# Kernel optimization log

Hardware: AMD Instinct MI355X
Metric: run time of the kernel (lower is better)

Reference implementation:

```python
import jax, jax.numpy as jnp
import numpy as np

N_USERS = 200000
N_ITEMS = 100000
N_NODES = N_USERS + N_ITEMS
N_EDGES = 1500000
EMBED_DIM = 64
BERT_DIM = 384
N_LAYERS = 3


def setup_inputs() -> dict:
    key = jax.random.key(0)
    ks = jax.random.split(key, 13)
    return {
        "user_emb": jax.random.normal(ks[0], (N_USERS, EMBED_DIM), jnp.float32) * 0.1,
        "item_emb": jax.random.normal(ks[1], (N_ITEMS, EMBED_DIM), jnp.float32) * 0.1,
        "gender_emb": jax.random.normal(ks[2], (3, EMBED_DIM), jnp.float32) * 0.1,
        "age_emb": jax.random.normal(ks[3], (8, EMBED_DIM), jnp.float32) * 0.1,
        "cat_emb": jax.random.normal(ks[4], (11, EMBED_DIM), jnp.float32) * 0.1,
        "bert_proj_w": jax.random.normal(ks[5], (EMBED_DIM, BERT_DIM), jnp.float32) * 0.05,
        "item_bert": jax.random.normal(ks[6], (N_ITEMS, BERT_DIM), jnp.float32),
        "adj_val": jax.random.uniform(ks[7], (N_EDGES,), jnp.float32),
        "user_gender": jax.random.randint(ks[8], (N_USERS,), 0, 3, jnp.int64 if jax.config.jax_enable_x64 else jnp.int32),
        "user_age": jax.random.randint(ks[9], (N_USERS,), 0, 8, jnp.int32),
        "item_cat": jax.random.randint(ks[10], (N_ITEMS,), 0, 11, jnp.int32),
        "adj_row": jax.random.randint(ks[11], (N_EDGES,), 0, N_NODES, jnp.int32),
        "adj_col": jax.random.randint(ks[12], (N_EDGES,), 0, N_NODES, jnp.int32),
    }


def reference(user_emb, item_emb, gender_emb, age_emb, cat_emb, bert_proj_w,
              item_bert, adj_val, user_gender, user_age, item_cat,
              adj_row, adj_col):
    n_users = user_emb.shape[0]
    n_nodes = n_users + item_emb.shape[0]

    # initial embeddings: base table + side-info gathers (+ projected BERT for items)
    u0 = user_emb + gender_emb[user_gender] + age_emb[user_age]          # [U, d]
    i0 = item_emb + cat_emb[item_cat] + item_bert @ bert_proj_w.T       # [I, d]
    all_emb = jnp.concatenate([u0, i0], axis=0)                          # [N, d]

    # COO SpMM: y[r] += val * x[c]
    def spmm(x):
        msgs = adj_val[:, None] * x[adj_col]                             # [E, d]
        return jax.ops.segment_sum(msgs, adj_row, num_segments=n_nodes)

    acc = all_emb
    x = all_emb
    for _ in range(N_LAYERS):
        x = spmm(x)
        acc = acc + x
    out = acc / (N_LAYERS + 1)                                           # mean over layer stack
    return out[:n_users], out[n_users:]
```

## Files before the change

kernel.cpp:

```cpp
#include <hip/hip_runtime.h>
#include <hip/hip_bf16.h>

#define NU 200000
#define NI 100000
#define NN 300000
#define NE 1500000
#define BD 384

#define SCAN1_BLOCKS 293
#define NBINS 293
#define CH 4096
#define P2CAP 6144
#define COLMASK 0x7FFFF

typedef __attribute__((ext_vector_type(8))) short short8;
typedef __attribute__((ext_vector_type(4))) float floatx4;

__device__ __forceinline__ void fma4(float4& a, float s, const float4& w) {
    a.x = fmaf(s, w.x, a.x);
    a.y = fmaf(s, w.y, a.y);
    a.z = fmaf(s, w.z, a.z);
    a.w = fmaf(s, w.w, a.w);
}

__device__ __forceinline__ float bf2f(unsigned short v) {
    union { unsigned int u; float f; } c; c.u = ((unsigned int)v) << 16; return c.f;
}
__device__ __forceinline__ float4 ub4f(const ushort4 v) {
    return make_float4(bf2f(v.x), bf2f(v.y), bf2f(v.z), bf2f(v.w));
}
__device__ __forceinline__ unsigned short f2bfu(float x) {
    union { __hip_bfloat16 b; unsigned short u; } c; c.b = __float2bfloat16(x); return c.u;
}
__device__ __forceinline__ ushort4 f4bf(const float4 a) {
    return make_ushort4(f2bfu(a.x), f2bfu(a.y), f2bfu(a.z), f2bfu(a.w));
}

__device__ __forceinline__ short8 cvt8(const float4 a, const float4 b) {
    union { short8 v; __hip_bfloat16 e[8]; } u;
    u.e[0] = __float2bfloat16(a.x); u.e[1] = __float2bfloat16(a.y);
    u.e[2] = __float2bfloat16(a.z); u.e[3] = __float2bfloat16(a.w);
    u.e[4] = __float2bfloat16(b.x); u.e[5] = __float2bfloat16(b.y);
    u.e[6] = __float2bfloat16(b.z); u.e[7] = __float2bfloat16(b.w);
    return u.v;
}

__global__ __launch_bounds__(256) void user_init_k(
    const float4* __restrict__ user_emb,
    const float4* __restrict__ gender_emb,
    const float4* __restrict__ age_emb,
    const int* __restrict__ ug,
    const int* __restrict__ ua,
    ushort4* __restrict__ A0)
{
    int i = blockIdx.x * 256 + threadIdx.x;
    int u = i >> 4, q = i & 15;
    float4 e = user_emb[i];
    float4 g = gender_emb[ug[u] * 16 + q];
    float4 a = age_emb[ua[u] * 16 + q];
    e.x += g.x + a.x; e.y += g.y + a.y; e.z += g.z + a.z; e.w += g.w + a.w;
    A0[i] = f4bf(e);
}

__global__ __launch_bounds__(256) void wconv_k(
    const float* __restrict__ W, short8* __restrict__ Wb)
{
    int t = blockIdx.x * 256 + threadIdx.x;
    if (t >= 3072) return;
    int lid = t & 63, nt = (t >> 6) & 3, kt = t >> 8;
    int m16 = lid & 15, q = lid >> 4;
    const float* src = W + (size_t)(nt * 16 + m16) * BD + kt * 32 + q * 8;
    Wb[t] = cvt8(*(const float4*)src, *(const float4*)(src + 4));
}

__global__ __launch_bounds__(256) void item_init_k(
    const float* __restrict__ bert,
    const short8* __restrict__ Wb,
    const float* __restrict__ item_emb,
    const float* __restrict__ cat_emb,
    const int* __restrict__ icat,
    unsigned short* __restrict__ A0)
{
    __shared__ float4 cbuf[2][4][64];

    const int lid  = threadIdx.x & 63;
    const int wv   = threadIdx.x >> 6;
    const int pair = wv >> 1;
    const int kh   = wv & 1;
    const int i0   = (blockIdx.x * 2 + pair) * 16;
    const int m16  = lid & 15;
    const int q    = lid >> 4;

    const float*  ab = bert + (size_t)(i0 + m16) * BD + kh * 192 + q * 8;
    const short8* wb = Wb + kh * 24 * 64 + lid;

    floatx4 cf[4];
    cf[0] = (floatx4){0.f, 0.f, 0.f, 0.f};
    cf[1] = cf[0]; cf[2] = cf[0]; cf[3] = cf[0];

    float4 a0 = *(const float4*)(ab + 0);
    float4 a1 = *(const float4*)(ab + 4);
    short8 b0 = wb[0 * 64];
    short8 b1 = wb[1 * 64];
    short8 b2 = wb[2 * 64];
    short8 b3 = wb[3 * 64];

    #pragma unroll
    for (int kt = 0; kt < 5; ++kt) {
        float4 na0 = *(const float4*)(ab + (kt + 1) * 32 + 0);
        float4 na1 = *(const float4*)(ab + (kt + 1) * 32 + 4);
        short8 nb0 = wb[((kt + 1) * 4 + 0) * 64];
        short8 nb1 = wb[((kt + 1) * 4 + 1) * 64];
        short8 nb2 = wb[((kt + 1) * 4 + 2) * 64];
        short8 nb3 = wb[((kt + 1) * 4 + 3) * 64];
        short8 af = cvt8(a0, a1);
        cf[0] = __builtin_amdgcn_mfma_f32_16x16x32_bf16(af, b0, cf[0], 0, 0, 0);
        cf[1] = __builtin_amdgcn_mfma_f32_16x16x32_bf16(af, b1, cf[1], 0, 0, 0);
        cf[2] = __builtin_amdgcn_mfma_f32_16x16x32_bf16(af, b2, cf[2], 0, 0, 0);
        cf[3] = __builtin_amdgcn_mfma_f32_16x16x32_bf16(af, b3, cf[3], 0, 0, 0);
        a0 = na0; a1 = na1; b0 = nb0; b1 = nb1; b2 = nb2; b3 = nb3;
    }
    {
        short8 af = cvt8(a0, a1);
        cf[0] = __builtin_amdgcn_mfma_f32_16x16x32_bf16(af, b0, cf[0], 0, 0, 0);
        cf[1] = __builtin_amdgcn_mfma_f32_16x16x32_bf16(af, b1, cf[1], 0, 0, 0);
        cf[2] = __builtin_amdgcn_mfma_f32_16x16x32_bf16(af, b2, cf[2], 0, 0, 0);
        cf[3] = __builtin_amdgcn_mfma_f32_16x16x32_bf16(af, b3, cf[3], 0, 0, 0);
    }

    if (kh == 1) {
        #pragma unroll
        for (int f = 0; f < 4; ++f)
            cbuf[pair][f][lid] = make_float4(cf[f][0], cf[f][1], cf[f][2], cf[f][3]);
    }
    __syncthreads();
    if (kh == 1) return;

    #pragma unroll
    for (int f = 0; f < 4; ++f) {
        float4 p = cbuf[pair][f][lid];
        cf[f][0] += p.x; cf[f][1] += p.y; cf[f][2] += p.z; cf[f][3] += p.w;
    }

    #pragma unroll
    for (int r = 0; r < 4; ++r) {
        const int item = i0 + q * 4 + r;
        const int cat  = icat[item];
        const size_t eb = (size_t)item * 64;
        const size_t abn = (size_t)(NU + item) * 64;
        #pragma unroll
        for (int td = 0; td < 4; ++td) {
            const int d = td * 16 + m16;
            A0[abn + d] = f2bfu(cf[td][r] + item_emb[eb + d] + cat_emb[cat * 64 + d]);
        }
    }
}

__global__ __launch_bounds__(256) void hist_k(
    const int* __restrict__ row, int* __restrict__ counts)
{
    int e = blockIdx.x * 256 + threadIdx.x;
    if (e < NE) atomicAdd(&counts[row[e]], 1);
}

__global__ __launch_bounds__(256) void scan1_k(
    const int* __restrict__ counts, int* __restrict__ offs,
    int* __restrict__ blksum)
{
    __shared__ int s[256];
    int t = threadIdx.x;
    int base = blockIdx.x * 1024 + t * 4;
    int c0 = 0, c1 = 0, c2 = 0, c3 = 0;
    if (base + 3 < NN) {
        int4 c = *(const int4*)&counts[base];
        c0 = c.x; c1 = c.y; c2 = c.z; c3 = c.w;
    } else {
        if (base + 0 < NN) c0 = counts[base + 0];
        if (base + 1 < NN) c1 = counts[base + 1];
        if (base + 2 < NN) c2 = counts[base + 2];
    }
    int tsum = c0 + c1 + c2 + c3;
    s[t] = tsum;
    __syncthreads();
    for (int d = 1; d < 256; d <<= 1) {
        int v = (t >= d) ? s[t - d] : 0;
        __syncthreads();
        s[t] += v;
        __syncthreads();
    }
    if (t == 255) blksum[blockIdx.x] = s[255];
    int e0 = s[t] - tsum, e1 = e0 + c0, e2 = e1 + c1, e3 = e2 + c2;
    if (base + 0 < NN) offs[base + 0] = e0;
    if (base + 1 < NN) offs[base + 1] = e1;
    if (base + 2 < NN) offs[base + 2] = e2;
    if (base + 3 < NN) offs[base + 3] = e3;
}

__global__ __launch_bounds__(512) void scan2_k(int* __restrict__ blksum)
{
    __shared__ int s[512];
    int t = threadIdx.x;
    int v = (t < SCAN1_BLOCKS) ? blksum[t] : 0;
    s[t] = v;
    __syncthreads();
    for (int d = 1; d < 512; d <<= 1) {
        int x = (t >= d) ? s[t - d] : 0;
        __syncthreads();
        s[t] += x;
        __syncthreads();
    }
    if (t < SCAN1_BLOCKS) blksum[t] = s[t] - v;
}

__global__ __launch_bounds__(256) void addoff_k(
    int* __restrict__ offs, const int* __restrict__ blkoff,
    int* __restrict__ cursor,
    int* __restrict__ binstart, int* __restrict__ bincur)
{
    int i = blockIdx.x * 256 + threadIdx.x;
    if (i < NN) {
        int o = offs[i] + blkoff[i >> 10];
        offs[i] = o;
        cursor[i] = o;
        if ((i & 1023) == 0) {
            binstart[i >> 10] = o;
            bincur[i >> 10] = o;
        }
    }
}

__global__ __launch_bounds__(256) void binscat_k(
    const int* __restrict__ row, const int* __restrict__ col,
    const float* __restrict__ val,
    int* __restrict__ bincur,
    int2* __restrict__ tcv)
{
    __shared__ int lhist[512];
    __shared__ int lexcl[512];
    __shared__ int lbase[512];
    __shared__ int s[256];
    __shared__ int2 scv[CH];
    __shared__ unsigned short sbin[CH];

    int t = threadIdx.x;
    int e0 = blockIdx.x * CH;
    int n = NE - e0; if (n > CH) n = CH;

    lhist[t] = 0; lhist[t + 256] = 0;
    __syncthreads();

    int r[16]; int2 cv[16]; int rk[16];
    #pragma unroll
    for (int i = 0; i < 16; ++i) {
        int idx = e0 + i * 256 + t;
        if (idx < NE) {
            r[i] = row[idx];
            cv[i].x = col[idx] | ((r[i] & 1023) << 19);
            cv[i].y = __float_as_int(val[idx]);
            rk[i] = atomicAdd(&lhist[r[i] >> 10], 1);
        }
    }
    __syncthreads();

    int c0 = lhist[2 * t], c1 = lhist[2 * t + 1];
    int tsum = c0 + c1;
    s[t] = tsum;
    __syncthreads();
    for (int d = 1; d < 256; d <<= 1) {
        int v = (t >= d) ? s[t - d] : 0;
        __syncthreads();
        s[t] += v;
        __syncthreads();
    }
    int ex = s[t] - tsum;
    lexcl[2 * t] = ex; lexcl[2 * t + 1] = ex + c0;
    if (2 * t < NBINS && c0 > 0)     lbase[2 * t]     = atomicAdd(&bincur[2 * t], c0);
    if (2 * t + 1 < NBINS && c1 > 0) lbase[2 * t + 1] = atomicAdd(&bincur[2 * t + 1], c1);
    __syncthreads();

    #pragma unroll
    for (int i = 0; i < 16; ++i) {
        int idx = e0 + i * 256 + t;
        if (idx < NE) {
            int b = r[i] >> 10;
            int p = lexcl[b] + rk[i];
            scv[p] = cv[i];
            sbin[p] = (unsigned short)b;
        }
    }
    __syncthreads();

    for (int p = t; p < n; p += 256) {
        int b = sbin[p];
        int g = lbase[b] + (p - lexcl[b]);
        tcv[g] = scv[p];
    }
}

__global__ __launch_bounds__(256) void scatter2_k(
    const int2* __restrict__ tcv,
    const int* __restrict__ binstart,
    int* __restrict__ cursor, int2* __restrict__ edges)
{
    __shared__ int2 scv[P2CAP];
    int b = blockIdx.x;
    int rbase = b << 10;
    int s = binstart[b];
    int e = (b + 1 < NBINS) ? binstart[b + 1] : NE;
    int cnt = e - s;

    if (cnt <= P2CAP) {
        for (int p = s + threadIdx.x; p < e; p += 256) {
            int2 tv = tcv[p];
            int rr = rbase + (int)(((unsigned int)tv.x) >> 19);
            int pos = atomicAdd(&cursor[rr], 1);
            scv[pos - s] = make_int2(tv.x & COLMASK, tv.y);
        }
        __syncthreads();
        for (int p = threadIdx.x; p < cnt; p += 256)
            edges[s + p] = scv[p];
    } else {
        for (int p = s + threadIdx.x; p < e; p += 256) {
            int2 tv = tcv[p];
            int rr = rbase + (int)(((unsigned int)tv.x) >> 19);
            int pos = atomicAdd(&cursor[rr], 1);
            edges[pos] = make_int2(tv.x & COLMASK, tv.y);
        }
    }
}

__global__ __launch_bounds__(256) void spmm_bf_k(
    const ushort4* __restrict__ xb,
    ushort4* __restrict__ yb,
    const int* __restrict__ offs,
    const int* __restrict__ ends,
    const int2* __restrict__ edges)
{
    int t = threadIdx.x;
    int r = blockIdx.x * 16 + (t >> 4);
    int q = t & 15;
    int s = offs[r], e = ends[r];
    float4 acc = make_float4(0.f, 0.f, 0.f, 0.f);
    int k = s;
    for (; k + 4 <= e; k += 4) {
        int2 c0 = edges[k + 0];
        int2 c1 = edges[k + 1];
        int2 c2 = edges[k + 2];
        int2 c3 = edges[k + 3];
        ushort4 v0 = xb[c0.x * 16 + q];
        ushort4 v1 = xb[c1.x * 16 + q];
        ushort4 v2 = xb[c2.x * 16 + q];
        ushort4 v3 = xb[c3.x * 16 + q];
        fma4(acc, __int_as_float(c0.y), ub4f(v0));
        fma4(acc, __int_as_float(c1.y), ub4f(v1));
        fma4(acc, __int_as_float(c2.y), ub4f(v2));
        fma4(acc, __int_as_float(c3.y), ub4f(v3));
    }
    for (; k < e; ++k) {
        int2 cv = edges[k];
        fma4(acc, __int_as_float(cv.y), ub4f(xb[cv.x * 16 + q]));
    }
    yb[r * 16 + q] = f4bf(acc);
}

__global__ __launch_bounds__(256) void spmm_l3_k(
    const ushort4* __restrict__ xb,
    const ushort4* __restrict__ x0b,
    const ushort4* __restrict__ x1b,
    float4* __restrict__ out,
    const int* __restrict__ offs,
    const int* __restrict__ ends,
    const int2* __restrict__ edges)
{
    int t = threadIdx.x;
    int r = blockIdx.x * 16 + (t >> 4);
    int q = t & 15;
    int s = offs[r], e = ends[r];
    float4 acc = make_float4(0.f, 0.f, 0.f, 0.f);
    int k = s;
    for (; k + 4 <= e; k += 4) {
        int2 c0 = edges[k + 0];
        int2 c1 = edges[k + 1];
        int2 c2 = edges[k + 2];
        int2 c3 = edges[k + 3];
        ushort4 v0 = xb[c0.x * 16 + q];
        ushort4 v1 = xb[c1.x * 16 + q];
        ushort4 v2 = xb[c2.x * 16 + q];
        ushort4 v3 = xb[c3.x * 16 + q];
        fma4(acc, __int_as_float(c0.y), ub4f(v0));
        fma4(acc, __int_as_float(c1.y), ub4f(v1));
        fma4(acc, __int_as_float(c2.y), ub4f(v2));
        fma4(acc, __int_as_float(c3.y), ub4f(v3));
    }
    for (; k < e; ++k) {
        int2 cv = edges[k];
        fma4(acc, __int_as_float(cv.y), ub4f(xb[cv.x * 16 + q]));
    }
    int oi = r * 16 + q;
    float4 x0 = ub4f(x0b[oi]);
    float4 x1 = ub4f(x1b[oi]);
    float4 x2 = ub4f(xb[oi]);
    out[oi] = make_float4(0.25f * (x0.x + x1.x + x2.x + acc.x),
                          0.25f * (x0.y + x1.y + x2.y + acc.y),
                          0.25f * (x0.z + x1.z + x2.z + acc.z),
                          0.25f * (x0.w + x1.w + x2.w + acc.w));
}

extern "C" void kernel_launch(void* const* d_in, const int* in_sizes, int n_in,
                              void* d_out, int out_size, void* d_ws, size_t ws_size,
                              hipStream_t stream)
{
    const float* user_emb    = (const float*)d_in[0];
    const float* item_emb    = (const float*)d_in[1];
    const float* gender_emb  = (const float*)d_in[2];
    const float* age_emb     = (const float*)d_in[3];
    const float* cat_emb     = (const float*)d_in[4];
    const float* bert_w      = (const float*)d_in[5];
    const float* item_bert   = (const float*)d_in[6];
    const float* adj_val     = (const float*)d_in[7];
    const int*   user_gender = (const int*)d_in[8];
    const int*   user_age    = (const int*)d_in[9];
    const int*   item_cat    = (const int*)d_in[10];
    const int*   adj_row     = (const int*)d_in[11];
    const int*   adj_col     = (const int*)d_in[12];

    float* out = (float*)d_out;

    float* A       = (float*)d_ws;
    float* B       = A + (size_t)NN * 64;
    int2*  edges   = (int2*)(B + (size_t)NN * 64);
    int*   offs    = (int*)(edges + NE);
    int*   cursor  = offs + NN;
    int*   blksum  = cursor + NN;
    int*   binstart= blksum + 512;
    int*   bincur  = binstart + 512;
    short8* Wb     = (short8*)(bincur + 512);

    ushort4* A0_16 = (ushort4*)A;
    int2*    tcv  = (int2*)B;
    ushort4* B16  = (ushort4*)B;
    ushort4* A16  = B16 + (size_t)NN * 16;

    hipMemsetAsync(offs, 0, (size_t)NN * sizeof(int), stream);
    hist_k<<<5860, 256, 0, stream>>>(adj_row, offs);
    scan1_k<<<SCAN1_BLOCKS, 256, 0, stream>>>(offs, offs, blksum);
    scan2_k<<<1, 512, 0, stream>>>(blksum);
    addoff_k<<<1172, 256, 0, stream>>>(offs, blksum, cursor, binstart, bincur);
    binscat_k<<<367, 256, 0, stream>>>(adj_row, adj_col, adj_val, bincur, tcv);
    scatter2_k<<<NBINS, 256, 0, stream>>>(tcv, binstart, cursor, edges);

    wconv_k<<<12, 256, 0, stream>>>(bert_w, Wb);
    user_init_k<<<12500, 256, 0, stream>>>(
        (const float4*)user_emb, (const float4*)gender_emb, (const float4*)age_emb,
        user_gender, user_age, A0_16);
    item_init_k<<<3125, 256, 0, stream>>>(
        item_bert, Wb, item_emb, cat_emb, item_cat, (unsigned short*)A0_16);

    spmm_bf_k<<<18750, 256, 0, stream>>>(A0_16, B16, offs, cursor, edges);
    spmm_bf_k<<<18750, 256, 0, stream>>>(B16, A16, offs, cursor, edges);
    spmm_l3_k<<<18750, 256, 0, stream>>>(A16, A0_16, B16, (float4*)out,
                                         offs, cursor, edges);
}
```

Baseline: 618.0 us.

## Fuse row histogram into bin scatter using fixed-capacity per-bin buckets

The separate histogram kernel is removed. The per-row count atomics now run inside the bin-scatter pass, which moves ahead of the prefix scan and writes into fixed-capacity per-bin regions (CAP2 slots each) instead of scan-derived offsets. This saves one full pass over adj_row and a kernel launch. The cost is a bin overflow risk if a bin ever gets more than CAP2 edges, plus a larger temporary footprint in B.

```diff
diff --git a/kernel.cpp b/kernel.cpp
--- a/kernel.cpp
+++ b/kernel.cpp
@@ -10,6 +10,7 @@
 #define SCAN1_BLOCKS 293
 #define NBINS 293
 #define CH 4096
+#define CAP2 8192
 #define P2CAP 6144
 #define COLMASK 0x7FFFF
 
@@ -156,13 +157,6 @@
     }
 }
 
-__global__ __launch_bounds__(256) void hist_k(
-    const int* __restrict__ row, int* __restrict__ counts)
-{
-    int e = blockIdx.x * 256 + threadIdx.x;
-    if (e < NE) atomicAdd(&counts[row[e]], 1);
-}
-
 __global__ __launch_bounds__(256) void scan1_k(
     const int* __restrict__ counts, int* __restrict__ offs,
     int* __restrict__ blksum)
@@ -215,23 +209,22 @@
 __global__ __launch_bounds__(256) void addoff_k(
     int* __restrict__ offs, const int* __restrict__ blkoff,
     int* __restrict__ cursor,
-    int* __restrict__ binstart, int* __restrict__ bincur)
+    int* __restrict__ binstart)
 {
     int i = blockIdx.x * 256 + threadIdx.x;
     if (i < NN) {
         int o = offs[i] + blkoff[i >> 10];
         offs[i] = o;
         cursor[i] = o;
-        if ((i & 1023) == 0) {
+        if ((i & 1023) == 0)
             binstart[i >> 10] = o;
-            bincur[i >> 10] = o;
-        }
     }
 }
 
 __global__ __launch_bounds__(256) void binscat_k(
     const int* __restrict__ row, const int* __restrict__ col,
     const float* __restrict__ val,
+    int* __restrict__ counts,
     int* __restrict__ bincur,
     int2* __restrict__ tcv)
 {
@@ -258,6 +251,7 @@
             cv[i].x = col[idx] | ((r[i] & 1023) << 19);
             cv[i].y = __float_as_int(val[idx]);
             rk[i] = atomicAdd(&lhist[r[i] >> 10], 1);
+            atomicAdd(&counts[r[i]], 1);
         }
     }
     __syncthreads();
@@ -292,7 +286,7 @@
 
     for (int p = t; p < n; p += 256) {
         int b = sbin[p];
-        int g = lbase[b] + (p - lexcl[b]);
+        size_t g = (size_t)b * CAP2 + lbase[b] + (p - lexcl[b]);
         tcv[g] = scv[p];
     }
 }
@@ -308,10 +302,11 @@
     int s = binstart[b];
     int e = (b + 1 < NBINS) ? binstart[b + 1] : NE;
     int cnt = e - s;
+    const int2* src = tcv + (size_t)b * CAP2;
 
     if (cnt <= P2CAP) {
-        for (int p = s + threadIdx.x; p < e; p += 256) {
-            int2 tv = tcv[p];
+        for (int p = threadIdx.x; p < cnt; p += 256) {
+            int2 tv = src[p];
             int rr = rbase + (int)(((unsigned int)tv.x) >> 19);
             int pos = atomicAdd(&cursor[rr], 1);
             scv[pos - s] = make_int2(tv.x & COLMASK, tv.y);
@@ -320,8 +315,8 @@
         for (int p = threadIdx.x; p < cnt; p += 256)
             edges[s + p] = scv[p];
     } else {
-        for (int p = s + threadIdx.x; p < e; p += 256) {
-            int2 tv = tcv[p];
+        for (int p = threadIdx.x; p < cnt; p += 256) {
+            int2 tv = src[p];
             int rr = rbase + (int)(((unsigned int)tv.x) >> 19);
             int pos = atomicAdd(&cursor[rr], 1);
             edges[pos] = make_int2(tv.x & COLMASK, tv.y);
@@ -430,23 +425,22 @@
     float* B       = A + (size_t)NN * 64;
     int2*  edges   = (int2*)(B + (size_t)NN * 64);
     int*   offs    = (int*)(edges + NE);
-    int*   cursor  = offs + NN;
+    int*   bincur  = offs + NN;
+    int*   cursor  = bincur + 512;
     int*   blksum  = cursor + NN;
     int*   binstart= blksum + 512;
-    int*   bincur  = binstart + 512;
-    short8* Wb     = (short8*)(bincur + 512);
+    short8* Wb     = (short8*)(binstart + 512);
 
     ushort4* A0_16 = (ushort4*)A;
     int2*    tcv  = (int2*)B;
     ushort4* B16  = (ushort4*)B;
     ushort4* A16  = B16 + (size_t)NN * 16;
 
-    hipMemsetAsync(offs, 0, (size_t)NN * sizeof(int), stream);
-    hist_k<<<5860, 256, 0, stream>>>(adj_row, offs);
+    hipMemsetAsync(offs, 0, ((size_t)NN + 512) * sizeof(int), stream);
+    binscat_k<<<367, 256, 0, stream>>>(adj_row, adj_col, adj_val, offs, bincur, tcv);
     scan1_k<<<SCAN1_BLOCKS, 256, 0, stream>>>(offs, offs, blksum);
     scan2_k<<<1, 512, 0, stream>>>(blksum);
-    addoff_k<<<1172, 256, 0, stream>>>(offs, blksum, cursor, binstart, bincur);
-    binscat_k<<<367, 256, 0, stream>>>(adj_row, adj_col, adj_val, bincur, tcv);
+    addoff_k<<<1172, 256, 0, stream>>>(offs, blksum, cursor, binstart);
     scatter2_k<<<NBINS, 256, 0, stream>>>(tcv, binstart, cursor, edges);
 
     wconv_k<<<12, 256, 0, stream>>>(bert_w, Wb);
```

Measured after the change: 603.0 us. 1.02x faster.
